# Kernel optimization log

Measured on AMD Instinct MI355X. Metric: run time of the kernel, lower is better.

Reference implementation:

```python
import jax, jax.numpy as jnp
from jax import lax
import numpy as np

SCALE = 1.0   # self.scale
EPS = 1e-12
CHUNK = 512   # points processed per chunk to bound [P,T,3] temporaries


def _closest_sqdist(p, a, b, c):
    """Squared distance from points p:[P,3] to triangles (a,b,c):[T,3] -> [P,T].
    Ericson's closest-point-on-triangle, fully vectorized."""
    ab = b - a
    ac = c - a
    bc = c - b
    ap = p[:, None, :] - a[None, :, :]
    bp = p[:, None, :] - b[None, :, :]
    cp = p[:, None, :] - c[None, :, :]
    d1 = jnp.einsum('td,ptd->pt', ab, ap)
    d2 = jnp.einsum('td,ptd->pt', ac, ap)
    d3 = jnp.einsum('td,ptd->pt', ab, bp)
    d4 = jnp.einsum('td,ptd->pt', ac, bp)
    d5 = jnp.einsum('td,ptd->pt', ab, cp)
    d6 = jnp.einsum('td,ptd->pt', ac, cp)
    va = d3 * d6 - d5 * d4
    vb = d5 * d2 - d1 * d6
    vc = d1 * d4 - d3 * d2

    def sdiv(n, d):  # NaN/Inf-safe division (branch is masked out by where anyway)
        return n / jnp.where(jnp.abs(d) < EPS, 1.0, d)

    t_ab = sdiv(d1, d1 - d3)[..., None]
    t_ac = sdiv(d2, d2 - d6)[..., None]
    t_bc = sdiv(d4 - d3, (d4 - d3) + (d5 - d6))[..., None]
    denom = va + vb + vc
    v_in = sdiv(vb, denom)[..., None]
    w_in = sdiv(vc, denom)[..., None]

    # base case: interior of the face; then overwrite with edge / vertex regions
    cl = a[None] + v_in * ab[None] + w_in * ac[None]
    cl = jnp.where(((va <= 0) & (d4 - d3 >= 0) & (d5 - d6 >= 0))[..., None],
                   b[None] + t_bc * bc[None], cl)   # edge BC
    cl = jnp.where(((vb <= 0) & (d2 >= 0) & (d6 <= 0))[..., None],
                   a[None] + t_ac * ac[None], cl)   # edge AC
    cl = jnp.where(((vc <= 0) & (d1 >= 0) & (d3 <= 0))[..., None],
                   a[None] + t_ab * ab[None], cl)   # edge AB
    cl = jnp.where(((d6 >= 0) & (d5 <= d6))[..., None], c[None], cl)  # vertex C
    cl = jnp.where(((d3 >= 0) & (d4 <= d3))[..., None], b[None], cl)  # vertex B
    cl = jnp.where(((d1 <= 0) & (d2 <= 0))[..., None], a[None], cl)   # vertex A
    diff = p[:, None, :] - cl
    return jnp.sum(diff * diff, axis=-1)


def setup_inputs():
    key = jax.random.key(0)
    k1, k2, k3 = jax.random.split(key, 3)
    vertices = jax.random.normal(k1, (4, 3, 16, 16, 16), dtype=jnp.float32)
    pc = jax.random.uniform(k2, (4, 4096, 3), dtype=jnp.float32)
    faces = jax.random.randint(k3, (8192, 3), 0, 4096, dtype=jnp.int32)
    return {"vertices": vertices, "pc": pc, "faces": faces}


def reference(vertices, pc, faces):
    B = vertices.shape[0]
    v = jax.nn.sigmoid(vertices)                     # self.normalization
    pos = jnp.moveaxis(v, 1, -1).reshape(B, -1, 3)   # permute(1,2,3,0).view(-1,3)
    pts = pc * SCALE                                 # _scale_points
    # pymesh path drops all-zero points; emulate with a mask (scaling keeps zeros zero)
    mask = jnp.any(pc != 0.0, axis=-1).astype(pts.dtype)  # [B,N]

    def per_batch(args):
        posb, pb, mb = args
        a = posb[faces[:, 0]]
        b = posb[faces[:, 1]]
        c = posb[faces[:, 2]]
        n_chunks = pb.shape[0] // CHUNK

        def chunk_min(pch):  # [CHUNK,3] -> [CHUNK] nearest sq-dist over all tris
            return jnp.min(_closest_sqdist(pch, a, b, c), axis=-1)

        d = lax.map(chunk_min, pb.reshape(n_chunks, CHUNK, 3)).reshape(-1)
        cnt = jnp.maximum(jnp.sum(mb), 1.0)
        return jnp.sum(d * mb) / cnt                 # mean(squared_distances)

    losses = lax.map(per_batch, (pos, pts, mask))    # [B]
    return jnp.mean(losses)
```

## Files before the change

### kernel.cpp

```cpp
#include <hip/hip_runtime.h>
#include <math.h>
#include <float.h>

#define NB 4
#define NP 4096
#define NT 8192
#define TREC 24
#define EPSD 1e-12
#define WNS 8
#define WTCH 64
#define WTOT (WNS*WTCH)
#define MNS 16
#define MTCH ((NT - WTOT)/MNS)

__device__ __forceinline__ float sigm(float x) { return 1.0f / (1.0f + expf(-x)); }

__device__ __forceinline__ float tri_dist(
    float px, float py, float pz,
    float ax, float ay, float az,
    float abx, float aby, float abz,
    float acx, float acy, float acz,
    float aa, float am, float cc,
    float raa, float rcc, float rbb,
    float rden, float den, float bb, float k1)
{
  float apx = px - ax, apy = py - ay, apz = pz - az;
  float d1   = apx*abx + apy*aby + apz*abz;
  float d2   = apx*acx + apy*acy + apz*acz;
  float apap = apx*apx + apy*apy + apz*apz;
  float vb = d1*cc - d2*am;
  float vc = d2*aa - d1*am;
  float va = den - vb - vc;
  float di = apap - (vb*d1 + vc*d2)*rden;
  float t2 = d1 + d1;
  float tab = fminf(fmaxf(d1*raa, 0.0f), 1.0f);
  float dAB = apap + tab*(tab*aa - t2);
  float t4 = d2 + d2;
  float tac = fminf(fmaxf(d2*rcc, 0.0f), 1.0f);
  float dAC = apap + tac*(tac*cc - t4);
  float e   = d2 - d1 + k1;
  float tbc = fminf(fmaxf(e*rbb, 0.0f), 1.0f);
  float distB = apap - t2 + aa;
  float dBC = distB + tbc*(tbc*bb - (e + e));
  float m3 = fminf(fminf(dAB, dAC), dBC);
  bool in = (vb >= 0.0f) & (vc >= 0.0f) & (va > 0.0f);
  return in ? di : m3;
}

__global__ __launch_bounds__(256) void prep_kernel(
    const float* __restrict__ verts, const int* __restrict__ faces,
    float* __restrict__ tri)
{
  int idx = blockIdx.x * 256 + threadIdx.x;
  if (idx >= NB * NT) return;
  int b = idx >> 13;
  int t = idx & (NT - 1);
  int f0 = faces[3*t + 0], f1 = faces[3*t + 1], f2i = faces[3*t + 2];
  const float* vb_ = verts + (size_t)b * 3 * NP;
  float ax = sigm(vb_[f0]),  ay = sigm(vb_[NP + f0]),  az = sigm(vb_[2*NP + f0]);
  float bx = sigm(vb_[f1]),  by = sigm(vb_[NP + f1]),  bz = sigm(vb_[2*NP + f1]);
  float cx = sigm(vb_[f2i]), cy = sigm(vb_[NP + f2i]), cz = sigm(vb_[2*NP + f2i]);
  float abx = bx - ax, aby = by - ay, abz = bz - az;
  float acx = cx - ax, acy = cy - ay, acz = cz - az;
  double aa = (double)abx*abx + (double)aby*aby + (double)abz*abz;
  double am = (double)abx*acx + (double)aby*acy + (double)abz*acz;
  double cc = (double)acx*acx + (double)acy*acy + (double)acz*acz;
  double den = aa*cc - am*am;
  double bb  = aa - 2.0*am + cc;
  float raa  = (fabs(aa)  < EPSD) ? 1.0f : (float)(1.0/aa);
  float rcc  = (fabs(cc)  < EPSD) ? 1.0f : (float)(1.0/cc);
  float rbb  = (fabs(bb)  < EPSD) ? 1.0f : (float)(1.0/bb);
  float rden = (fabs(den) < EPSD) ? 0.0f : (float)(1.0/den);
  double nx = (double)aby*acz - (double)abz*acy;
  double ny = (double)abz*acx - (double)abx*acz;
  double nz = (double)abx*acy - (double)aby*acx;
  double na = nx*ax + ny*ay + nz*az;
  float denadj = (fabs(den) < EPSD) ? 1e30f : (float)(den * 1.02);
  float* r = tri + (size_t)idx * TREC;
  r[0]  = (float)nx; r[1]  = (float)ny; r[2]  = (float)nz; r[3] = (float)(-na);
  r[4]  = denadj;    r[5]  = ax;        r[6]  = ay;        r[7] = az;
  r[8]  = abx;       r[9]  = aby;       r[10] = abz;       r[11] = acx;
  r[12] = acy;       r[13] = acz;       r[14] = (float)aa; r[15] = (float)am;
  r[16] = (float)cc; r[17] = raa;       r[18] = rcc;       r[19] = rbb;
  r[20] = rden;      r[21] = (float)den;r[22] = (float)bb; r[23] = (float)(aa - am);
}

__global__ __launch_bounds__(256) void warm_kernel(
    const float* __restrict__ tri, const float* __restrict__ pc,
    float* __restrict__ partW)
{
  int bid  = blockIdx.x;
  int pblk = bid & 15;
  int s    = (bid >> 4) & (WNS - 1);
  int b    = bid >> 7;
  int p    = pblk * 256 + threadIdx.x;
  const float* pp = pc + ((size_t)b * NP + p) * 3;
  float px = pp[0], py = pp[1], pz = pp[2];
  const float4* R = (const float4*)(tri + ((size_t)b * NT + s * WTCH) * TREC);
  float mind = FLT_MAX;
  float4 h1 = R[1], h2 = R[2], h3 = R[3], h4 = R[4], h5 = R[5];
  for (int t = 0; t < WTCH; ++t) {
    const float4* Rn = R + 6;
    float4 g1 = Rn[1], g2 = Rn[2], g3 = Rn[3], g4 = Rn[4], g5 = Rn[5];
    float dd = tri_dist(px, py, pz,
                        h1.y, h1.z, h1.w,
                        h2.x, h2.y, h2.z,
                        h2.w, h3.x, h3.y,
                        h3.z, h3.w, h4.x,
                        h4.y, h4.z, h4.w,
                        h5.x, h5.y, h5.z, h5.w);
    mind = fminf(mind, dd);
    h1 = g1; h2 = g2; h3 = g3; h4 = g4; h5 = g5;
    R = Rn;
  }
  partW[((size_t)b * WNS + s) * NP + p] = fmaxf(mind, 0.0f);
}

__global__ __launch_bounds__(256) void main_kernel(
    const float* __restrict__ tri, const float* __restrict__ pc,
    const float* __restrict__ partW, float* __restrict__ partM)
{
  __shared__ unsigned qbuf[4][128];
  __shared__ unsigned wmind[4][64];

  int bid  = blockIdx.x;
  int pblk = bid & 15;
  int s    = (bid >> 4) & (MNS - 1);
  int b    = bid >> 8;
  int tid  = threadIdx.x;
  int wave = tid >> 6, lane = tid & 63;
  int p    = pblk * 256 + tid;

  const float* pp = pc + ((size_t)b * NP + p) * 3;
  float px = pp[0], py = pp[1], pz = pp[2];

  float mind = FLT_MAX;
  #pragma unroll
  for (int j = 0; j < WNS; ++j)
    mind = fminf(mind, partW[((size_t)b * WNS + j) * NP + p]);
  wmind[wave][lane] = __float_as_uint(mind);

  unsigned qcnt = 0u, qd = 0u;
  const float* triB = tri + (size_t)b * NT * TREC;
  int tg0 = WTOT + s * MTCH;
  const float4* Rf = (const float4*)(triB + (size_t)tg0 * TREC);

#define DRAIN_BATCH(NACT)                                                     \
  {                                                                           \
    unsigned ent = qbuf[wave][(qd + (unsigned)lane) & 127u];                  \
    if ((unsigned)lane < (unsigned)(NACT)) {                                  \
      int te  = (int)(ent >> 6);                                              \
      int src = (int)(ent & 63u);                                             \
      float qx = __shfl(px, src, 64);                                         \
      float qy = __shfl(py, src, 64);                                         \
      float qz = __shfl(pz, src, 64);                                         \
      const float* rr = triB + (size_t)te * TREC;                             \
      float4 w1 = *(const float4*)(rr + 4);                                   \
      float4 w2 = *(const float4*)(rr + 8);                                   \
      float4 w3 = *(const float4*)(rr + 12);                                  \
      float4 w4 = *(const float4*)(rr + 16);                                  \
      float4 w5 = *(const float4*)(rr + 20);                                  \
      float dd = fmaxf(tri_dist(qx, qy, qz,                                   \
                                w1.y, w1.z, w1.w,                             \
                                w2.x, w2.y, w2.z,                             \
                                w2.w, w3.x, w3.y,                             \
                                w3.z, w3.w, w4.x,                             \
                                w4.y, w4.z, w4.w,                             \
                                w5.x, w5.y, w5.z, w5.w), 0.0f);               \
      atomicMin(&wmind[wave][src], __float_as_uint(dd));                      \
    }                                                                         \
    qd += (unsigned)(NACT);                                                   \
    mind = fminf(mind, __uint_as_float(wmind[wave][lane]));                   \
  }

#define SCAN_ITER(Q0, DA, TIDX)                                               \
  {                                                                           \
    float sN = fmaf(pz, (Q0).z, fmaf(py, (Q0).y, fmaf(px, (Q0).x, (Q0).w)));  \
    bool pred = (sN * sN) < (mind * (DA));                                    \
    unsigned long long mask = __ballot(pred);                                 \
    if (mask) {                                                               \
      if (pred) {                                                             \
        int prefix = __builtin_amdgcn_mbcnt_hi((unsigned)(mask >> 32),        \
                       __builtin_amdgcn_mbcnt_lo((unsigned)mask, 0));         \
        qbuf[wave][(qcnt + (unsigned)prefix) & 127u] =                        \
            ((unsigned)(TIDX) << 6) | (unsigned)lane;                         \
      }                                                                       \
      qcnt += (unsigned)__builtin_popcountll(mask);                           \
      if (qcnt - qd >= 64u) DRAIN_BATCH(64u);                                 \
    }                                                                         \
  }

  float4 c00 = Rf[0],  c01 = Rf[1],  c10 = Rf[6],  c11 = Rf[7];
  float4 c20 = Rf[12], c21 = Rf[13], c30 = Rf[18], c31 = Rf[19];
  int tg = tg0;
  for (int g = 0; g < MTCH / 4; ++g) {
    const float4* Rn = Rf + 24;
    float4 n00 = Rn[0],  n01 = Rn[1],  n10 = Rn[6],  n11 = Rn[7];
    float4 n20 = Rn[12], n21 = Rn[13], n30 = Rn[18], n31 = Rn[19];
    SCAN_ITER(c00, c01.x, tg + 0);
    SCAN_ITER(c10, c11.x, tg + 1);
    SCAN_ITER(c20, c21.x, tg + 2);
    SCAN_ITER(c30, c31.x, tg + 3);
    c00 = n00; c01 = n01; c10 = n10; c11 = n11;
    c20 = n20; c21 = n21; c30 = n30; c31 = n31;
    Rf = Rn; tg += 4;
  }

  unsigned pend = qcnt - qd;
  if (pend) DRAIN_BATCH(pend);
  mind = fminf(mind, __uint_as_float(wmind[wave][lane]));

  partM[((size_t)b * MNS + s) * NP + p] = fmaxf(mind, 0.0f);

#undef SCAN_ITER
#undef DRAIN_BATCH
}

__global__ __launch_bounds__(256) void reduce_kernel(
    const float* __restrict__ part, const float* __restrict__ pc,
    float* __restrict__ bl2)
{
  int blk = blockIdx.x;
  int b = blk >> 4;
  int p = (blk & 15) * 256 + threadIdx.x;
  float m = FLT_MAX;
  #pragma unroll
  for (int s = 0; s < MNS; ++s)
    m = fminf(m, part[((size_t)b * MNS + s) * NP + p]);
  const float* pp = pc + ((size_t)b * NP + p) * 3;
  float x = pp[0], y = pp[1], z = pp[2];
  float msk = ((x != 0.0f) | (y != 0.0f) | (z != 0.0f)) ? 1.0f : 0.0f;
  float sdm = m * msk, sm = msk;
  for (int off = 32; off > 0; off >>= 1) {
    sdm += __shfl_down(sdm, off, 64);
    sm  += __shfl_down(sm,  off, 64);
  }
  __shared__ float s1[4], s2[4];
  int wave = threadIdx.x >> 6, lanei = threadIdx.x & 63;
  if (lanei == 0) { s1[wave] = sdm; s2[wave] = sm; }
  __syncthreads();
  if (threadIdx.x == 0) {
    bl2[2 * blk]     = s1[0] + s1[1] + s1[2] + s1[3];
    bl2[2 * blk + 1] = s2[0] + s2[1] + s2[2] + s2[3];
  }
}

__global__ void final_kernel(const float* __restrict__ bl2, float* __restrict__ out)
{
  if (threadIdx.x == 0 && blockIdx.x == 0) {
    float acc = 0.0f;
    for (int b = 0; b < NB; ++b) {
      float sdm = 0.0f, sm = 0.0f;
      for (int k = 0; k < 16; ++k) {
        sdm += bl2[2 * (b * 16 + k)];
        sm  += bl2[2 * (b * 16 + k) + 1];
      }
      acc += sdm / fmaxf(sm, 1.0f);
    }
    out[0] = 0.25f * acc;
  }
}

extern "C" void kernel_launch(void* const* d_in, const int* in_sizes, int n_in,
                              void* d_out, int out_size, void* d_ws, size_t ws_size,
                              hipStream_t stream) {
  const float* verts = (const float*)d_in[0];
  const float* pc    = (const float*)d_in[1];
  const int*   faces = (const int*)d_in[2];
  float* out = (float*)d_out;

  float* tri   = (float*)d_ws;
  float* partW = tri   + (size_t)NB * NT * TREC;
  float* partM = partW + (size_t)NB * WNS * NP;
  float* bl2   = partM + (size_t)NB * MNS * NP;

  prep_kernel<<<(NB * NT) / 256, 256, 0, stream>>>(verts, faces, tri);
  warm_kernel<<<NB * WNS * 16, 256, 0, stream>>>(tri, pc, partW);
  main_kernel<<<NB * MNS * 16, 256, 0, stream>>>(tri, pc, partW, partM);
  reduce_kernel<<<NB * 16, 256, 0, stream>>>(partM, pc, bl2);
  final_kernel<<<1, 64, 0, stream>>>(bl2, out);
}
```

Measured before the change: 170.4 us.

## Seed bounds from vertex distances and add bounding-box triangle culling

Replaces the warm-up pass over the first 512 triangles with a cheap nearest-vertex pass. It computes sigmoid positions once and brute-forces point-to-vertex distances to seed each point's upper bound. The main scan now covers all triangles. It uses a normalized plane plus an axis-aligned bounding-box distance test to cull candidates, reading a compact 12-float scan record and a separate 20-float exact record. The vertex seed is only a valid upper bound for vertices that belong to some face, so unreferenced vertices can make the bound too small and corrupt results. The AABB test adds arithmetic to every scan step.

```diff
diff --git a/kernel.cpp b/kernel.cpp
--- a/kernel.cpp
+++ b/kernel.cpp
@@ -5,13 +5,13 @@
 #define NB 4
 #define NP 4096
 #define NT 8192
-#define TREC 24
+#define TSE 12
+#define TEE 20
 #define EPSD 1e-12
-#define WNS 8
-#define WTCH 64
-#define WTOT (WNS*WTCH)
-#define MNS 16
-#define MTCH ((NT - WTOT)/MNS)
+#define MNS 32
+#define MTCH (NT/MNS)
+#define VCH 16
+#define VLEN (NP/VCH)
 
 __device__ __forceinline__ float sigm(float x) { return 1.0f / (1.0f + expf(-x)); }
 
@@ -47,19 +47,26 @@
   return in ? di : m3;
 }
 
+__global__ __launch_bounds__(256) void vert_kernel(
+    const float* __restrict__ verts, float* __restrict__ pos)
+{
+  int i = blockIdx.x * 256 + threadIdx.x;
+  if (i < NB * 3 * NP) pos[i] = sigm(verts[i]);
+}
+
 __global__ __launch_bounds__(256) void prep_kernel(
-    const float* __restrict__ verts, const int* __restrict__ faces,
-    float* __restrict__ tri)
+    const float* __restrict__ pos, const int* __restrict__ faces,
+    float* __restrict__ triS, float* __restrict__ triE)
 {
   int idx = blockIdx.x * 256 + threadIdx.x;
   if (idx >= NB * NT) return;
   int b = idx >> 13;
   int t = idx & (NT - 1);
   int f0 = faces[3*t + 0], f1 = faces[3*t + 1], f2i = faces[3*t + 2];
-  const float* vb_ = verts + (size_t)b * 3 * NP;
-  float ax = sigm(vb_[f0]),  ay = sigm(vb_[NP + f0]),  az = sigm(vb_[2*NP + f0]);
-  float bx = sigm(vb_[f1]),  by = sigm(vb_[NP + f1]),  bz = sigm(vb_[2*NP + f1]);
-  float cx = sigm(vb_[f2i]), cy = sigm(vb_[NP + f2i]), cz = sigm(vb_[2*NP + f2i]);
+  const float* pb = pos + (size_t)b * 3 * NP;
+  float ax = pb[f0],  ay = pb[NP + f0],  az = pb[2*NP + f0];
+  float bx = pb[f1],  by = pb[NP + f1],  bz = pb[2*NP + f1];
+  float cx = pb[f2i], cy = pb[NP + f2i], cz = pb[2*NP + f2i];
   float abx = bx - ax, aby = by - ay, abz = bz - az;
   float acx = cx - ax, acy = cy - ay, acz = cz - az;
   double aa = (double)abx*abx + (double)aby*aby + (double)abz*abz;
@@ -74,51 +81,67 @@
   double nx = (double)aby*acz - (double)abz*acy;
   double ny = (double)abz*acx - (double)abx*acz;
   double nz = (double)abx*acy - (double)aby*acx;
-  double na = nx*ax + ny*ay + nz*az;
-  float denadj = (fabs(den) < EPSD) ? 1e30f : (float)(den * 1.02);
-  float* r = tri + (size_t)idx * TREC;
-  r[0]  = (float)nx; r[1]  = (float)ny; r[2]  = (float)nz; r[3] = (float)(-na);
-  r[4]  = denadj;    r[5]  = ax;        r[6]  = ay;        r[7] = az;
-  r[8]  = abx;       r[9]  = aby;       r[10] = abz;       r[11] = acx;
-  r[12] = acy;       r[13] = acz;       r[14] = (float)aa; r[15] = (float)am;
-  r[16] = (float)cc; r[17] = raa;       r[18] = rcc;       r[19] = rbb;
-  r[20] = rden;      r[21] = (float)den;r[22] = (float)bb; r[23] = (float)(aa - am);
-}
-
-__global__ __launch_bounds__(256) void warm_kernel(
-    const float* __restrict__ tri, const float* __restrict__ pc,
-    float* __restrict__ partW)
+  double rs = (fabs(den) < EPSD) ? 0.0 : 1.0 / sqrt(den * 1.02);
+  float nhx = (float)(nx * rs), nhy = (float)(ny * rs), nhz = (float)(nz * rs);
+  float w = (float)(-(nx*ax + ny*ay + nz*az) * rs);
+  float lox = fminf(ax, fminf(bx, cx)), hix = fmaxf(ax, fmaxf(bx, cx));
+  float loy = fminf(ay, fminf(by, cy)), hiy = fmaxf(ay, fmaxf(by, cy));
+  float loz = fminf(az, fminf(bz, cz)), hiz = fmaxf(az, fmaxf(bz, cz));
+  float* rs_ = triS + (size_t)idx * TSE;
+  rs_[0] = nhx; rs_[1] = nhy; rs_[2] = nhz; rs_[3]  = w;
+  rs_[4] = lox; rs_[5] = loy; rs_[6] = loz; rs_[7]  = hix;
+  rs_[8] = hiy; rs_[9] = hiz; rs_[10] = 0.0f; rs_[11] = 0.0f;
+  float* re = triE + (size_t)idx * TEE;
+  re[0]  = ax;  re[1]  = ay;  re[2]  = az;  re[3]  = abx;
+  re[4]  = aby; re[5]  = abz; re[6]  = acx; re[7]  = acy;
+  re[8]  = acz; re[9]  = (float)aa; re[10] = (float)am; re[11] = (float)cc;
+  re[12] = raa; re[13] = rcc; re[14] = rbb; re[15] = rden;
+  re[16] = (float)den; re[17] = (float)bb; re[18] = (float)(aa - am); re[19] = 0.0f;
+}
+
+__global__ __launch_bounds__(256) void seed_kernel(
+    const float* __restrict__ pos, const float* __restrict__ pc,
+    float* __restrict__ partS)
 {
   int bid  = blockIdx.x;
   int pblk = bid & 15;
-  int s    = (bid >> 4) & (WNS - 1);
-  int b    = bid >> 7;
+  int vc   = (bid >> 4) & (VCH - 1);
+  int b    = bid >> 8;
   int p    = pblk * 256 + threadIdx.x;
   const float* pp = pc + ((size_t)b * NP + p) * 3;
   float px = pp[0], py = pp[1], pz = pp[2];
-  const float4* R = (const float4*)(tri + ((size_t)b * NT + s * WTCH) * TREC);
-  float mind = FLT_MAX;
-  float4 h1 = R[1], h2 = R[2], h3 = R[3], h4 = R[4], h5 = R[5];
-  for (int t = 0; t < WTCH; ++t) {
-    const float4* Rn = R + 6;
-    float4 g1 = Rn[1], g2 = Rn[2], g3 = Rn[3], g4 = Rn[4], g5 = Rn[5];
-    float dd = tri_dist(px, py, pz,
-                        h1.y, h1.z, h1.w,
-                        h2.x, h2.y, h2.z,
-                        h2.w, h3.x, h3.y,
-                        h3.z, h3.w, h4.x,
-                        h4.y, h4.z, h4.w,
-                        h5.x, h5.y, h5.z, h5.w);
-    mind = fminf(mind, dd);
-    h1 = g1; h2 = g2; h3 = g3; h4 = g4; h5 = g5;
-    R = Rn;
-  }
-  partW[((size_t)b * WNS + s) * NP + p] = fmaxf(mind, 0.0f);
+  const float* base = pos + (size_t)b * 3 * NP + vc * VLEN;
+  const float4* X = (const float4*)(base);
+  const float4* Y = (const float4*)(base + NP);
+  const float4* Z = (const float4*)(base + 2 * NP);
+  float m = FLT_MAX;
+  #pragma unroll 4
+  for (int v = 0; v < VLEN / 4; ++v) {
+    float4 vx = X[v], vy = Y[v], vz = Z[v];
+    {
+      float dx = px - vx.x, dy = py - vy.x, dz = pz - vz.x;
+      m = fminf(m, dx*dx + dy*dy + dz*dz);
+    }
+    {
+      float dx = px - vx.y, dy = py - vy.y, dz = pz - vz.y;
+      m = fminf(m, dx*dx + dy*dy + dz*dz);
+    }
+    {
+      float dx = px - vx.z, dy = py - vy.z, dz = pz - vz.z;
+      m = fminf(m, dx*dx + dy*dy + dz*dz);
+    }
+    {
+      float dx = px - vx.w, dy = py - vy.w, dz = pz - vz.w;
+      m = fminf(m, dx*dx + dy*dy + dz*dz);
+    }
+  }
+  partS[((size_t)b * VCH + vc) * NP + p] = m;
 }
 
 __global__ __launch_bounds__(256) void main_kernel(
-    const float* __restrict__ tri, const float* __restrict__ pc,
-    const float* __restrict__ partW, float* __restrict__ partM)
+    const float* __restrict__ triS, const float* __restrict__ triE,
+    const float* __restrict__ pc, const float* __restrict__ partS,
+    float* __restrict__ partM)
 {
   __shared__ unsigned qbuf[4][128];
   __shared__ unsigned wmind[4][64];
@@ -126,7 +149,7 @@
   int bid  = blockIdx.x;
   int pblk = bid & 15;
   int s    = (bid >> 4) & (MNS - 1);
-  int b    = bid >> 8;
+  int b    = bid >> 9;
   int tid  = threadIdx.x;
   int wave = tid >> 6, lane = tid & 63;
   int p    = pblk * 256 + tid;
@@ -136,14 +159,15 @@
 
   float mind = FLT_MAX;
   #pragma unroll
-  for (int j = 0; j < WNS; ++j)
-    mind = fminf(mind, partW[((size_t)b * WNS + j) * NP + p]);
+  for (int j = 0; j < VCH; ++j)
+    mind = fminf(mind, partS[((size_t)b * VCH + j) * NP + p]);
   wmind[wave][lane] = __float_as_uint(mind);
+  float mth = mind + 1e-8f;
 
   unsigned qcnt = 0u, qd = 0u;
-  const float* triB = tri + (size_t)b * NT * TREC;
-  int tg0 = WTOT + s * MTCH;
-  const float4* Rf = (const float4*)(triB + (size_t)tg0 * TREC);
+  const float* triEB = triE + (size_t)b * NT * TEE;
+  int tg0 = s * MTCH;
+  const float4* Rs = (const float4*)(triS + (size_t)(b * NT + tg0) * TSE);
 
 #define DRAIN_BATCH(NACT)                                                     \
   {                                                                           \
@@ -154,29 +178,34 @@
       float qx = __shfl(px, src, 64);                                         \
       float qy = __shfl(py, src, 64);                                         \
       float qz = __shfl(pz, src, 64);                                         \
-      const float* rr = triB + (size_t)te * TREC;                             \
-      float4 w1 = *(const float4*)(rr + 4);                                   \
-      float4 w2 = *(const float4*)(rr + 8);                                   \
-      float4 w3 = *(const float4*)(rr + 12);                                  \
-      float4 w4 = *(const float4*)(rr + 16);                                  \
-      float4 w5 = *(const float4*)(rr + 20);                                  \
+      const float* rr = triEB + (size_t)te * TEE;                             \
+      float4 w1 = *(const float4*)(rr + 0);                                   \
+      float4 w2 = *(const float4*)(rr + 4);                                   \
+      float4 w3 = *(const float4*)(rr + 8);                                   \
+      float4 w4 = *(const float4*)(rr + 12);                                  \
+      float4 w5 = *(const float4*)(rr + 16);                                  \
       float dd = fmaxf(tri_dist(qx, qy, qz,                                   \
-                                w1.y, w1.z, w1.w,                             \
-                                w2.x, w2.y, w2.z,                             \
-                                w2.w, w3.x, w3.y,                             \
-                                w3.z, w3.w, w4.x,                             \
-                                w4.y, w4.z, w4.w,                             \
-                                w5.x, w5.y, w5.z, w5.w), 0.0f);               \
+                                w1.x, w1.y, w1.z,                             \
+                                w1.w, w2.x, w2.y,                             \
+                                w2.z, w2.w, w3.x,                             \
+                                w3.y, w3.z, w3.w,                             \
+                                w4.x, w4.y, w4.z,                             \
+                                w4.w, w5.x, w5.y, w5.z), 0.0f);               \
       atomicMin(&wmind[wave][src], __float_as_uint(dd));                      \
     }                                                                         \
     qd += (unsigned)(NACT);                                                   \
     mind = fminf(mind, __uint_as_float(wmind[wave][lane]));                   \
-  }
-
-#define SCAN_ITER(Q0, DA, TIDX)                                               \
+    mth  = mind + 1e-8f;                                                      \
+  }
+
+#define SCAN_ITER(Q0, Q1, Q2, TIDX)                                           \
   {                                                                           \
     float sN = fmaf(pz, (Q0).z, fmaf(py, (Q0).y, fmaf(px, (Q0).x, (Q0).w)));  \
-    bool pred = (sN * sN) < (mind * (DA));                                    \
+    float dx = fmaxf(fmaxf((Q1).x - px, px - (Q1).w), 0.0f);                  \
+    float dy = fmaxf(fmaxf((Q1).y - py, py - (Q2).x), 0.0f);                  \
+    float dz = fmaxf(fmaxf((Q1).z - pz, pz - (Q2).y), 0.0f);                  \
+    float bb2 = dx*dx + dy*dy + dz*dz;                                        \
+    bool pred = (sN * sN < mth) & (bb2 * 0.98f < mth);                        \
     unsigned long long mask = __ballot(pred);                                 \
     if (mask) {                                                               \
       if (pred) {                                                             \
@@ -190,20 +219,18 @@
     }                                                                         \
   }
 
-  float4 c00 = Rf[0],  c01 = Rf[1],  c10 = Rf[6],  c11 = Rf[7];
-  float4 c20 = Rf[12], c21 = Rf[13], c30 = Rf[18], c31 = Rf[19];
+  float4 a0 = Rs[0], a1 = Rs[1], a2 = Rs[2];
+  float4 b0 = Rs[3], b1 = Rs[4], b2 = Rs[5];
   int tg = tg0;
-  for (int g = 0; g < MTCH / 4; ++g) {
-    const float4* Rn = Rf + 24;
-    float4 n00 = Rn[0],  n01 = Rn[1],  n10 = Rn[6],  n11 = Rn[7];
-    float4 n20 = Rn[12], n21 = Rn[13], n30 = Rn[18], n31 = Rn[19];
-    SCAN_ITER(c00, c01.x, tg + 0);
-    SCAN_ITER(c10, c11.x, tg + 1);
-    SCAN_ITER(c20, c21.x, tg + 2);
-    SCAN_ITER(c30, c31.x, tg + 3);
-    c00 = n00; c01 = n01; c10 = n10; c11 = n11;
-    c20 = n20; c21 = n21; c30 = n30; c31 = n31;
-    Rf = Rn; tg += 4;
+  for (int g = 0; g < MTCH / 2; ++g) {
+    const float4* Rn = Rs + 6;
+    float4 c0 = Rn[0], c1 = Rn[1], c2 = Rn[2];
+    float4 d0 = Rn[3], d1 = Rn[4], d2 = Rn[5];
+    SCAN_ITER(a0, a1, a2, tg + 0);
+    SCAN_ITER(b0, b1, b2, tg + 1);
+    a0 = c0; a1 = c1; a2 = c2;
+    b0 = d0; b1 = d1; b2 = d2;
+    Rs = Rn; tg += 2;
   }
 
   unsigned pend = qcnt - qd;
@@ -269,14 +296,17 @@
   const int*   faces = (const int*)d_in[2];
   float* out = (float*)d_out;
 
-  float* tri   = (float*)d_ws;
-  float* partW = tri   + (size_t)NB * NT * TREC;
-  float* partM = partW + (size_t)NB * WNS * NP;
+  float* pos   = (float*)d_ws;
+  float* triS  = pos   + (size_t)NB * 3 * NP;
+  float* triE  = triS  + (size_t)NB * NT * TSE;
+  float* partS = triE  + (size_t)NB * NT * TEE;
+  float* partM = partS + (size_t)NB * VCH * NP;
   float* bl2   = partM + (size_t)NB * MNS * NP;
 
-  prep_kernel<<<(NB * NT) / 256, 256, 0, stream>>>(verts, faces, tri);
-  warm_kernel<<<NB * WNS * 16, 256, 0, stream>>>(tri, pc, partW);
-  main_kernel<<<NB * MNS * 16, 256, 0, stream>>>(tri, pc, partW, partM);
+  vert_kernel<<<(NB * 3 * NP) / 256, 256, 0, stream>>>(verts, pos);
+  prep_kernel<<<(NB * NT) / 256, 256, 0, stream>>>(pos, faces, triS, triE);
+  seed_kernel<<<NB * VCH * 16, 256, 0, stream>>>(pos, pc, partS);
+  main_kernel<<<NB * MNS * 16, 256, 0, stream>>>(triS, triE, pc, partS, partM);
   reduce_kernel<<<NB * 16, 256, 0, stream>>>(partM, pc, bl2);
   final_kernel<<<1, 64, 0, stream>>>(bl2, out);
 }
```

Measured after the change: 164.4 us. 3.5% less time.
